# Kernel tuning notes

Hardware: AMD Instinct MI355X
Metric: run time of the kernel (lower is better)

## Reference

```python
import jax, jax.numpy as jnp
import numpy as np

L, N, E, D, H = 3, 20000, 320000, 128, 4
EPS = 1.1920929e-07  # torch RMSNorm default eps = finfo(float32).eps
NEG_SLOPE = 0.2      # PyG GATConv leaky_relu negative_slope


def rmsnorm(x, w):
    return x * jax.lax.rsqrt(jnp.mean(x * x, axis=-1, keepdims=True) + EPS) * w


def setup_inputs() -> dict:
    key = jax.random.key(0)
    ks = jax.random.split(key, 13)
    s = 0.02
    x = jax.random.normal(ks[0], (N, D), jnp.float32)
    src = jax.random.randint(ks[1], (E,), 0, N, dtype=jnp.int64)
    dst = jax.random.randint(ks[2], (E,), 0, N, dtype=jnp.int64)
    dst = jnp.where(dst == src, (dst + 1) % N, dst)  # no pre-existing self loops
    edge_index = jnp.stack([src, dst])
    return {
        "x": x,
        "W_gat": jax.random.normal(ks[3], (L, D, H * D), jnp.float32) * s,
        "att_src": jax.random.normal(ks[4], (L, H, D), jnp.float32) * s,
        "att_dst": jax.random.normal(ks[5], (L, H, D), jnp.float32) * s,
        "bias_gat": jax.random.normal(ks[6], (L, D), jnp.float32) * s,
        "W1": jax.random.normal(ks[7], (L, D, D), jnp.float32) * s,
        "b1": jax.random.normal(ks[8], (L, D), jnp.float32) * s,
        "W2": jax.random.normal(ks[9], (L, D, D), jnp.float32) * s,
        "b2": jax.random.normal(ks[10], (L, D), jnp.float32) * s,
        "norm1_w": jnp.ones((L, D), jnp.float32),
        "norm2_w": jnp.ones((L, D), jnp.float32),
        "edge_index": edge_index,
    }


def reference(x, W_gat, att_src, att_dst, bias_gat, W1, b1, W2, b2, norm1_w, norm2_w, edge_index):
    # PyG GATConv adds self loops by default
    loops = jnp.arange(N, dtype=edge_index.dtype)
    src = jnp.concatenate([edge_index[0], loops])  # [E+N]
    dst = jnp.concatenate([edge_index[1], loops])
    for i in range(L):
        # --- GATConv(hidden, hidden, heads=H, concat=False), dropout=0 (eval) ---
        xp = (x @ W_gat[i]).reshape(N, H, D)               # [N,H,D]
        a_s = jnp.einsum('nhd,hd->nh', xp, att_src[i])     # [N,H]
        a_d = jnp.einsum('nhd,hd->nh', xp, att_dst[i])
        e = jax.nn.leaky_relu(a_s[src] + a_d[dst], NEG_SLOPE)  # [E+N,H]
        m = jax.ops.segment_max(e, dst, num_segments=N)
        ex = jnp.exp(e - m[dst])
        denom = jax.ops.segment_sum(ex, dst, num_segments=N)
        alpha = ex / denom[dst]                             # segment softmax over incoming edges
        agg = jax.ops.segment_sum(alpha[:, :, None] * xp[src], dst, num_segments=N)  # [N,H,D]
        x_att = agg.mean(axis=1) + bias_gat[i]              # concat=False -> head mean, then bias
        # --- residual + RMSNorm ---
        x = rmsnorm(x + x_att, norm1_w[i])
        # --- FFN ---
        h = jax.nn.relu(x @ W1[i] + b1[i])
        h = h @ W2[i] + b2[i]
        x = rmsnorm(x + h, norm2_w[i])
    return x
```

## Files before the change

kernel.cpp:

```cpp
#include <hip/hip_runtime.h>
#include <hip/hip_bf16.h>

#define N_NODES 20000
#define NEDGE   320000
#define DIM     128
#define NH      4
#define HD      512
#define LAYERS  3
#define EPS_RMS 1.1920929e-07f
#define SLOPE   0.2f
#define NTILES  (N_NODES >> 4)

#define NWGC  (LAYERS * DIM * HD)
#define NW1C  (LAYERS * DIM * DIM)
#define NVC   (LAYERS * DIM)
#define NPACK (NWGC + 2 * NW1C + 5 * NVC)
#define NXV   (N_NODES * DIM / 8)

typedef __bf16 bf16_t;
typedef __bf16 bf16v2 __attribute__((ext_vector_type(2)));
typedef __bf16 bf16v8 __attribute__((ext_vector_type(8)));
typedef float  f32v4  __attribute__((ext_vector_type(4)));
typedef float  f32v2  __attribute__((ext_vector_type(2)));

__device__ __forceinline__ int clamp_node(int s) {
    return ((unsigned)s >= (unsigned)N_NODES) ? 0 : s;
}
__device__ __forceinline__ float leaky(float e) { return e > 0.f ? e : SLOPE * e; }
__device__ __forceinline__ unsigned char enc_fp8(float v) {
    int p = __builtin_amdgcn_cvt_pk_fp8_f32(v, v, 0, false);
    return (unsigned char)(p & 0xff);
}
__device__ __forceinline__ unsigned short enc_fp8_pair(float a, float b) {
    int p = __builtin_amdgcn_cvt_pk_fp8_f32(a, b, 0, false);
    return (unsigned short)(p & 0xffff);
}

__device__ __forceinline__ bool wave_detect_bf16(const unsigned short* xh) {
    int lane = threadIdx.x & 63;
    unsigned short hw = xh[2 * lane];
    int e = (hw >> 7) & 0xff;
    unsigned long long b = __ballot(e >= 96 && e <= 140);
    return __popcll(b) >= 48;
}
__device__ __forceinline__ bool wave_detect_i64(const int* ei) {
    int lane = threadIdx.x & 63;
    unsigned long long b = __ballot(ei[2 * lane + 1] != 0);
    return b == 0ULL;
}
__device__ __forceinline__ float raw_elem(const void* in, size_t j, bool isbf) {
    return isbf ? (float)((const bf16_t*)in)[j] : ((const float*)in)[j];
}
__device__ __forceinline__ bf16_t cvt_elem(const void* in, size_t j, bool isbf) {
    return isbf ? ((const bf16_t*)in)[j] : (bf16_t)((const float*)in)[j];
}
__device__ __forceinline__ int edge_src(const int* ei, int e, bool is64) {
    return clamp_node(is64 ? ei[2 * e] : ei[e]);
}
__device__ __forceinline__ int edge_dst(const int* ei, int e, bool is64) {
    return clamp_node(is64 ? ei[2 * NEDGE + 2 * e] : ei[NEDGE + e]);
}

__global__ __launch_bounds__(256) void prep_v(const void* x, const void* Wg,
                                              const void* aS, const void* aD,
                                              float* __restrict__ vS, float* __restrict__ vD,
                                              int* __restrict__ deg) {
    int gid = blockIdx.x * 256 + threadIdx.x;
    for (int i = gid; i < N_NODES; i += gridDim.x * 256) deg[i] = 0;
    bool isbf = wave_detect_bf16((const unsigned short*)x);
    int w = gid >> 6;
    if (w >= LAYERS * DIM * NH * 2) return;
    int lane = threadIdx.x & 63;
    int sd = w & 1, h = (w >> 1) & 3, k = (w >> 3) & 127, l = w >> 10;
    const void* att = sd ? aD : aS;
    size_t wbase = (size_t)l * DIM * HD + (size_t)k * HD + h * DIM;
    size_t abase = (size_t)l * NH * DIM + (size_t)h * DIM;
    int c = 2 * lane;
    float p = raw_elem(Wg, wbase + c, isbf) * raw_elem(att, abase + c, isbf)
            + raw_elem(Wg, wbase + c + 1, isbf) * raw_elem(att, abase + c + 1, isbf);
#pragma unroll
    for (int msk = 1; msk < 64; msk <<= 1) p += __shfl_xor(p, msk);
    if (lane == 0) {
        float* dst = sd ? vD : vS;
        dst[l * HD + h * DIM + k] = p;
    }
}

__device__ __forceinline__ void pack_item(int i, bool isbf,
        const void* Wg, const void* W1, const void* W2,
        const void* bg, const void* b1, const void* b2,
        const void* n1, const void* n2,
        bf16_t* WmixP, bf16_t* W1P, bf16_t* W2P,
        bf16_t* bgc, bf16_t* b1c, bf16_t* b2c, bf16_t* n1c, bf16_t* n2c) {
    if (i < NWGC) {
        int l = i >> 16;
        int r = i & 65535;
        int j = r & 7;
        int lane2 = (r >> 3) & 63;
        int mm = lane2 & 15, kqq = lane2 >> 4;
        int tt = (r >> 9) & 1;
        int kk = (r >> 10) & 15;
        int wvv = r >> 14;
        int kidx = kk * 32 + kqq * 8 + j;
        int h = kidx >> 7, kp = kidx & 127;
        int c = 32 * wvv + tt * 16 + mm;
        WmixP[i] = cvt_elem(Wg, (size_t)l * DIM * HD + (size_t)kp * HD + h * DIM + c, isbf);
        return;
    }
    i -= NWGC;
    if (i < NW1C) {
        int l = i / 16384;
        int r = i & 16383;
        int j = r & 7;
        int lane2 = (r >> 3) & 63;
        int mm = lane2 & 15, kqq = lane2 >> 4;
        int tt = (r >> 9) & 1;
        int ks = (r >> 10) & 3;
        int wvv = r >> 12;
        int k = ks * 32 + kqq * 8 + j;
        int c = 32 * wvv + tt * 16 + mm;
        W1P[i] = cvt_elem(W1, (size_t)l * DIM * DIM + (size_t)k * DIM + c, isbf);
        return;
    }
    i -= NW1C;
    if (i < NW1C) {
        int l = i / 16384;
        int r = i & 16383;
        int j = r & 7;
        int lane2 = (r >> 3) & 63;
        int mm = lane2 & 15, kqq = lane2 >> 4;
        int tt = (r >> 9) & 1;
        int ks = (r >> 10) & 3;
        int wvv = r >> 12;
        int k = ks * 32 + kqq * 8 + j;
        int c = 32 * wvv + tt * 16 + mm;
        W2P[i] = cvt_elem(W2, (size_t)l * DIM * DIM + (size_t)k * DIM + c, isbf);
        return;
    }
    i -= NW1C;
    if (i >= 5 * NVC) return;
    int seg = i / NVC, k = i - seg * NVC;
    if (seg == 0) bgc[k] = cvt_elem(bg, k, isbf);
    else if (seg == 1) b1c[k] = cvt_elem(b1, k, isbf);
    else if (seg == 2) b2c[k] = cvt_elem(b2, k, isbf);
    else if (seg == 3) n1c[k] = cvt_elem(n1, k, isbf);
    else n2c[k] = cvt_elem(n2, k, isbf);
}

__global__ __launch_bounds__(256) void mega_setup(
        const void* x, const void* Wg, const void* W1, const void* W2,
        const void* bg, const void* b1, const void* b2, const void* n1, const void* n2,
        bf16_t* xb, bf16_t* WmixP, bf16_t* W1P, bf16_t* W2P,
        bf16_t* bgc, bf16_t* b1c, bf16_t* b2c, bf16_t* n1c, bf16_t* n2c,
        const int* ei, int* deg,
        const float* vS, const float* vD,
        float* a_s, float* a_d, unsigned short* x8,
        int convBlocks, int histBlocks) {
    int b = (int)blockIdx.x;
    if (b >= convBlocks + histBlocks) {
        bool isbf = wave_detect_bf16((const unsigned short*)x);
        int lane = threadIdx.x & 63;
        int n = (b - convBlocks - histBlocks) * 4 + (int)(threadIdx.x >> 6);
        if (n >= N_NODES) return;
        int c = 2 * lane;
        float f0 = raw_elem(x, (size_t)n * DIM + c, isbf);
        float f1 = raw_elem(x, (size_t)n * DIM + c + 1, isbf);
        x8[n * 64 + lane] = enc_fp8_pair(f0, f1);
#pragma unroll
        for (int h = 0; h < NH; ++h) {
            float ps = f0 * vS[h * DIM + c] + f1 * vS[h * DIM + c + 1];
            float pd = f0 * vD[h * DIM + c] + f1 * vD[h * DIM + c + 1];
#pragma unroll
            for (int msk = 1; msk < 64; msk <<= 1) {
                ps += __shfl_xor(ps, msk);
                pd += __shfl_xor(pd, msk);
            }
            if (lane == 0) {
                a_s[n * 4 + h] = ps;
                a_d[n * 4 + h] = pd;
            }
        }
        return;
    }
    if (b >= convBlocks) {
        bool is64 = wave_detect_i64(ei);
        int e = (b - convBlocks) * 256 + threadIdx.x;
        if (e < NEDGE) atomicAdd(&deg[edge_dst(ei, e, is64)], 1);
        return;
    }
    bool isbf = wave_detect_bf16((const unsigned short*)x);
    int i = b * 256 + threadIdx.x;
    if (i < NXV) {
        if (isbf) {
            ((bf16v8*)xb)[i] = ((const bf16v8*)x)[i];
        } else {
            const float4* src = (const float4*)x;
            float4 a = src[2 * i], bq = src[2 * i + 1];
            bf16v8 o;
            o[0] = (bf16_t)a.x;  o[1] = (bf16_t)a.y;
            o[2] = (bf16_t)a.z;  o[3] = (bf16_t)a.w;
            o[4] = (bf16_t)bq.x; o[5] = (bf16_t)bq.y;
            o[6] = (bf16_t)bq.z; o[7] = (bf16_t)bq.w;
            ((bf16v8*)xb)[i] = o;
        }
        return;
    }
    pack_item(i - NXV, isbf, Wg, W1, W2, bg, b1, b2, n1, n2,
              WmixP, W1P, W2P, bgc, b1c, b2c, n1c, n2c);
}

__global__ __launch_bounds__(1024) void scan_kernel(const int* __restrict__ deg,
                                                    int* __restrict__ row_ptr,
                                                    int* __restrict__ cursor) {
    __shared__ int wsum[16];
    int tid = threadIdx.x, lane = tid & 63, wv = tid >> 6;
    int v[20];
    int base = tid * 20;
    int tot = 0;
    if (base < N_NODES) {
        const int4* d4 = reinterpret_cast<const int4*>(deg + base);
#pragma unroll
        for (int j = 0; j < 5; ++j) {
            int4 q = d4[j];
            v[4 * j]     = q.x;
            v[4 * j + 1] = q.y;
            v[4 * j + 2] = q.z;
            v[4 * j + 3] = q.w;
        }
#pragma unroll
        for (int i = 0; i < 20; ++i) tot += v[i];
    }
    int x = tot;
#pragma unroll
    for (int off = 1; off < 64; off <<= 1) {
        int t = __shfl_up(x, off);
        if (lane >= off) x += t;
    }
    if (lane == 63) wsum[wv] = x;
    __syncthreads();
    if (wv == 0) {
        int s = (lane < 16) ? wsum[lane] : 0;
#pragma unroll
        for (int off = 1; off < 16; off <<= 1) {
            int t = __shfl_up(s, off);
            if (lane >= off) s += t;
        }
        if (lane < 16) wsum[lane] = s;
    }
    __syncthreads();
    int off0 = ((wv == 0) ? 0 : wsum[wv - 1]) + (x - tot);
    if (tid == 0) row_ptr[0] = 0;
    if (base < N_NODES) {
        int run = off0;
#pragma unroll
        for (int i = 0; i < 20; ++i) {
            run += v[i];
            row_ptr[base + i + 1] = run;
            cursor[base + i] = run - v[i];
        }
    }
}

__global__ void fill_kernel(const int* __restrict__ ei, int* __restrict__ cursor,
                            int* __restrict__ csr_src) {
    bool is64 = wave_detect_i64(ei);
    int e = blockIdx.x * blockDim.x + threadIdx.x;
    if (e < NEDGE) {
        int d = edge_dst(ei, e, is64);
        int pos = atomicAdd(&cursor[d], 1);
        if ((unsigned)pos < (unsigned)NEDGE) csr_src[pos] = edge_src(ei, e, is64);
    }
}

__device__ __forceinline__ void acc_group_loop(float (&acc)[8], int cnt,
        const float4* wshw, const int* sshw,
        const unsigned short* __restrict__ x8, int lane) {
    unsigned short xeN[8];
    {
        int p0 = cnt < 8 ? cnt : 8;
#pragma unroll
        for (int u = 0; u < 8; ++u)
            if (u < p0) xeN[u] = x8[sshw[u] + lane];
    }
    for (int u0 = 0; u0 < cnt; u0 += 8) {
        int uc = cnt - u0; if (uc > 8) uc = 8;
        unsigned short xeC[8];
#pragma unroll
        for (int u = 0; u < 8; ++u) xeC[u] = xeN[u];
        int n0 = u0 + 8;
        int nc = cnt - n0; if (nc > 8) nc = 8;
#pragma unroll
        for (int u = 0; u < 8; ++u)
            if (u < nc) xeN[u] = x8[sshw[n0 + u] + lane];
#pragma unroll
        for (int u = 0; u < 8; ++u) {
            if (u < uc) {
                float4 w = wshw[u0 + u];
                f32v2 f = __builtin_amdgcn_cvt_pk_f32_fp8((int)xeC[u], false);
                acc[0] += w.x * f[0]; acc[1] += w.x * f[1];
                acc[2] += w.y * f[0]; acc[3] += w.y * f[1];
                acc[4] += w.z * f[0]; acc[5] += w.z * f[1];
                acc[6] += w.w * f[0]; acc[7] += w.w * f[1];
            }
        }
    }
}

__device__ __forceinline__ void gat_phaseA(int tile, int wv, int lane,
        float4* wshw, int* sshw,
        const int* __restrict__ row_ptr, const int* __restrict__ csr_src,
        const float* __restrict__ a_s, const float* __restrict__ a_d,
        const unsigned short* __restrict__ x8, bf16_t (*ylds)[524]) {
    const float4* a_s4 = reinterpret_cast<const float4*>(a_s);
    const float4* a_d4 = reinterpret_cast<const float4*>(a_d);

    int beg[4], deg[4];
#pragma unroll
    for (int rp = 0; rp < 4; ++rp) {
        int nn = tile * 16 + wv + rp * 4;
        int b = row_ptr[nn], e = row_ptr[nn + 1];
        int d = e - b;
        if (d < 0) d = 0;
        if (d > NEDGE) d = NEDGE;
        if (b < 0) b = 0;
        if (b > NEDGE - d) b = NEDGE - d;
        beg[rp] = b; deg[rp] = d;
    }

    int craw[4], sreg[4];
    unsigned short pslf[4];
    float4 av4[4], adv4[4], avs4[4];

    {
        int d = deg[0];
        int idx = (d > 0) ? (beg[0] + (lane < d ? lane : 0)) : 0;
        craw[0] = csr_src[idx];
        d = deg[1];
        idx = (d > 0) ? (beg[1] + (lane < d ? lane : 0)) : 0;
        craw[1] = csr_src[idx];
        int nn = tile * 16 + wv;
        adv4[0] = a_d4[nn];
        avs4[0] = a_s4[nn];
        pslf[0] = x8[nn * 64 + lane];
        int s = clamp_node(craw[0]);
        sreg[0] = s;
        av4[0] = a_s4[s];
    }

#pragma unroll
    for (int rp = 0; rp < 4; ++rp) {
        float4 adv = adv4[rp];
        float4 a0 = av4[rp];
        float4 wl = {__expf(leaky(a0.x + adv.x)), __expf(leaky(a0.y + adv.y)),
                     __expf(leaky(a0.z + adv.z)), __expf(leaky(a0.w + adv.w))};
        float4 avs = avs4[rp];
        float4 wself = {__expf(leaky(avs.x + adv.x)), __expf(leaky(avs.y + adv.y)),
                        __expf(leaky(avs.z + adv.z)), __expf(leaky(avs.w + adv.w))};
        float acc[8];
        {
            f32v2 f = __builtin_amdgcn_cvt_pk_f32_fp8((int)pslf[rp], false);
            acc[0] = wself.x * f[0]; acc[1] = wself.x * f[1];
            acc[2] = wself.y * f[0]; acc[3] = wself.y * f[1];
            acc[4] = wself.z * f[0]; acc[5] = wself.z * f[1];
            acc[6] = wself.w * f[0]; acc[7] = wself.w * f[1];
        }
        int cnt0 = deg[rp] < 64 ? deg[rp] : 64;
        float4 zl = {0.f, 0.f, 0.f, 0.f};
        if (lane < cnt0) {
            zl = wl;
            wshw[lane] = wl;
            sshw[lane] = sreg[rp] << 6;
        }

        if (rp < 3) {
            int nn = tile * 16 + wv + (rp + 1) * 4;
            adv4[rp + 1] = a_d4[nn];
            avs4[rp + 1] = a_s4[nn];
            pslf[rp + 1] = x8[nn * 64 + lane];
            int s = clamp_node(craw[rp + 1]);
            sreg[rp + 1] = s;
            av4[rp + 1] = a_s4[s];
        }
        if (rp < 2) {
            int d = deg[rp + 2];
            int idx = (d > 0) ? (beg[rp + 2] + (lane < d ? lane : 0)) : 0;
            craw[rp + 2] = csr_src[idx];
        }

        acc_group_loop(acc, cnt0, wshw, sshw, x8, lane);

        for (int c0 = 64; c0 < deg[rp]; c0 += 64) {
            int cnt = deg[rp] - c0; if (cnt > 64) cnt = 64;
            if (lane < cnt) {
                int s = clamp_node(csr_src[beg[rp] + c0 + lane]);
                float4 a2 = a_s4[s];
                float4 w2 = {__expf(leaky(a2.x + adv.x)), __expf(leaky(a2.y + adv.y)),
                             __expf(leaky(a2.z + adv.z)), __expf(leaky(a2.w + adv.w))};
                zl.x += w2.x; zl.y += w2.y; zl.z += w2.z; zl.w += w2.w;
                wshw[lane] = w2;
                sshw[lane] = s << 6;
            }
            acc_group_loop(acc, cnt, wshw, sshw, x8, lane);
        }

        float4 zr = zl;
#pragma unroll
        for (int msk = 1; msk < 64; msk <<= 1) {
            zr.x += __shfl_xor(zr.x, msk);
            zr.y += __shfl_xor(zr.y, msk);
            zr.z += __shfl_xor(zr.z, msk);
            zr.w += __shfl_xor(zr.w, msk);
        }
        float4 z4 = {wself.x + zr.x, wself.y + zr.y, wself.z + zr.z, wself.w + zr.w};
        float4 ih4 = {1.f / z4.x, 1.f / z4.y, 1.f / z4.z, 1.f / z4.w};
        int c = 2 * lane;
        bf16_t* yrow = &ylds[wv + rp * 4][0];
#pragma unroll
        for (int h = 0; h < NH; ++h) {
            float ih = h == 0 ? ih4.x : h == 1 ? ih4.y : h == 2 ? ih4.z : ih4.w;
            bf16v2 o;
            o[0] = (bf16_t)(acc[h * 2 + 0] * ih);
            o[1] = (bf16_t)(acc[h * 2 + 1] * ih);
            *reinterpret_cast<bf16v2*>(&yrow[h * DIM + c]) = o;
        }
    }
}

template <int MODE>
__global__ __launch_bounds__(256) void gat_mix(
        const int* __restrict__ row_ptr, const int* __restrict__ csr_src,
        const float* __restrict__ a_s, const float* __restrict__ a_d,
        const unsigned short* __restrict__ x8,
        const bf16_t* __restrict__ WmixP, const bf16_t* __restrict__ bg,
        const bf16_t* __restrict__ n1w, const bf16_t* __restrict__ xb,
        const bf16_t* __restrict__ W1P, const bf16_t* __restrict__ b1,
        const bf16_t* __restrict__ W2P, const bf16_t* __restrict__ b2,
        const bf16_t* __restrict__ n2w, void* __restrict__ out,
        const float* __restrict__ vS, const float* __restrict__ vD,
        float* __restrict__ a_s_n, float* __restrict__ a_d_n,
        unsigned char* __restrict__ x8_n) {
    __shared__ bf16_t ylds[16][524];
    __shared__ bf16_t xm[16][140];
    __shared__ float  ssq_p[16][4];
    __shared__ float  asd_p[4][16][8];
    __shared__ float4 wsh[4][64];
    __shared__ int    ssh[4][64];
    bf16_t (*hh)[140] = reinterpret_cast<bf16_t (*)[140]>(&ylds[0][0]);

    int tile = blockIdx.x;
    int wv = threadIdx.x >> 6;
    int lane = threadIdx.x & 63;
    int m = lane & 15, kq = lane >> 4;

    gat_phaseA(tile, wv, lane, wsh[wv], ssh[wv], row_ptr, csr_src, a_s, a_d, x8, ylds);
    __syncthreads();

    f32v4 accm[2];
    accm[0] = (f32v4){0.f, 0.f, 0.f, 0.f};
    accm[1] = (f32v4){0.f, 0.f, 0.f, 0.f};
#pragma unroll
    for (int kk = 0; kk < 16; ++kk) {
        bf16v8 a = *reinterpret_cast<const bf16v8*>(&ylds[m][kk * 32 + kq * 8]);
#pragma unroll
        for (int tt = 0; tt < 2; ++tt) {
            bf16v8 b = *reinterpret_cast<const bf16v8*>(
                WmixP + ((((wv * 16 + kk) * 2 + tt) << 9) + lane * 8));
            accm[tt] = __builtin_amdgcn_mfma_f32_16x16x32_bf16(a, b, accm[tt], 0, 0, 0);
        }
    }
    float vals[2][4];
    {
        float sp[4] = {0.f, 0.f, 0.f, 0.f};
#pragma unroll
        for (int tt = 0; tt < 2; ++tt) {
            int col = 32 * wv + tt * 16 + m;
            float bv = (float)bg[col];
#pragma unroll
            for (int r = 0; r < 4; ++r) {
                int gr = tile * 16 + kq * 4 + r;
                float v = 0.25f * accm[tt][r] + bv + (float)xb[(size_t)gr * DIM + col];
                vals[tt][r] = v;
                sp[r] += v * v;
            }
        }
#pragma unroll
        for (int r = 0; r < 4; ++r) {
            sp[r] += __shfl_xor(sp[r], 1); sp[r] += __shfl_xor(sp[r], 2);
            sp[r] += __shfl_xor(sp[r], 4); sp[r] += __shfl_xor(sp[r], 8);
            if (m == r) ssq_p[kq * 4 + r][wv] = sp[r];
        }
    }
    __syncthreads();
    {
#pragma unroll
        for (int r = 0; r < 4; ++r) {
            int row = kq * 4 + r;
            float s = ssq_p[row][0] + ssq_p[row][1] + ssq_p[row][2] + ssq_p[row][3];
            float scale = rsqrtf(s * (1.f / 128.f) + EPS_RMS);
#pragma unroll
            for (int tt = 0; tt < 2; ++tt) {
                int col = 32 * wv + tt * 16 + m;
                xm[row][col] = (bf16_t)(vals[tt][r] * scale * (float)n1w[col]);
            }
        }
    }
    __syncthreads();

    f32v4 acc1[2];
    acc1[0] = (f32v4){0.f, 0.f, 0.f, 0.f};
    acc1[1] = (f32v4){0.f, 0.f, 0.f, 0.f};
#pragma unroll
    for (int ks = 0; ks < 4; ++ks) {
        bf16v8 a = *reinterpret_cast<const bf16v8*>(&xm[m][ks * 32 + kq * 8]);
#pragma unroll
        for (int tt = 0; tt < 2; ++tt) {
            bf16v8 b = *reinterpret_cast<const bf16v8*>(
                W1P + ((((wv * 4 + ks) * 2 + tt) << 9) + lane * 8));
            acc1[tt] = __builtin_amdgcn_mfma_f32_16x16x32_bf16(a, b, acc1[tt], 0, 0, 0);
        }
    }
#pragma unroll
    for (int tt = 0; tt < 2; ++tt) {
        int col = 32 * wv + tt * 16 + m;
        float bv = (float)b1[col];
#pragma unroll
        for (int r = 0; r < 4; ++r) {
            float v = acc1[tt][r] + bv;
            hh[kq * 4 + r][col] = (bf16_t)(v > 0.f ? v : 0.f);
        }
    }
    __syncthreads();
    f32v4 acc2[2];
    acc2[0] = (f32v4){0.f, 0.f, 0.f, 0.f};
    acc2[1] = (f32v4){0.f, 0.f, 0.f, 0.f};
#pragma unroll
    for (int ks = 0; ks < 4; ++ks) {
        bf16v8 a = *reinterpret_cast<const bf16v8*>(&hh[m][ks * 32 + kq * 8]);
#pragma unroll
        for (int tt = 0; tt < 2; ++tt) {
            bf16v8 b = *reinterpret_cast<const bf16v8*>(
                W2P + ((((wv * 4 + ks) * 2 + tt) << 9) + lane * 8));
            acc2[tt] = __builtin_amdgcn_mfma_f32_16x16x32_bf16(a, b, acc2[tt], 0, 0, 0);
        }
    }
    float vals2[2][4];
    {
        float sp[4] = {0.f, 0.f, 0.f, 0.f};
#pragma unroll
        for (int tt = 0; tt < 2; ++tt) {
            int col = 32 * wv + tt * 16 + m;
            float bv = (float)b2[col];
#pragma unroll
            for (int r = 0; r < 4; ++r) {
                float v = acc2[tt][r] + bv + (float)xm[kq * 4 + r][col];
                vals2[tt][r] = v;
                sp[r] += v * v;
            }
        }
#pragma unroll
        for (int r = 0; r < 4; ++r) {
            sp[r] += __shfl_xor(sp[r], 1); sp[r] += __shfl_xor(sp[r], 2);
            sp[r] += __shfl_xor(sp[r], 4); sp[r] += __shfl_xor(sp[r], 8);
            if (m == r) ssq_p[kq * 4 + r][wv] = sp[r];
        }
    }
    __syncthreads();
    float o2[2][4];
#pragma unroll
    for (int r = 0; r < 4; ++r) {
        int row = kq * 4 + r;
        int gr = tile * 16 + row;
        float s = ssq_p[row][0] + ssq_p[row][1] + ssq_p[row][2] + ssq_p[row][3];
        float scale = rsqrtf(s * (1.f / 128.f) + EPS_RMS);
#pragma unroll
        for (int tt = 0; tt < 2; ++tt) {
            int col = 32 * wv + tt * 16 + m;
            float o = vals2[tt][r] * scale * (float)n2w[col];
            o2[tt][r] = o;
            if (MODE == 1) ((float*)out)[(size_t)gr * DIM + col] = o;
            else {
                ((bf16_t*)out)[(size_t)gr * DIM + col] = (bf16_t)o;
                x8_n[(size_t)gr * DIM + col] = enc_fp8(o);
            }
        }
    }
    if (MODE == 0) {
        float vs0[NH], vs1[NH], vd0[NH], vd1[NH];
        int col0 = 32 * wv + m, col1 = col0 + 16;
#pragma unroll
        for (int h = 0; h < NH; ++h) {
            vs0[h] = vS[h * DIM + col0]; vs1[h] = vS[h * DIM + col1];
            vd0[h] = vD[h * DIM + col0]; vd1[h] = vD[h * DIM + col1];
        }
#pragma unroll
        for (int r = 0; r < 4; ++r) {
#pragma unroll
            for (int h = 0; h < NH; ++h) {
                float ps = o2[0][r] * vs0[h] + o2[1][r] * vs1[h];
                float pd = o2[0][r] * vd0[h] + o2[1][r] * vd1[h];
                ps += __shfl_xor(ps, 1); ps += __shfl_xor(ps, 2);
                ps += __shfl_xor(ps, 4); ps += __shfl_xor(ps, 8);
                pd += __shfl_xor(pd, 1); pd += __shfl_xor(pd, 2);
                pd += __shfl_xor(pd, 4); pd += __shfl_xor(pd, 8);
                if (m == r * 4 + h) {
                    asd_p[wv][kq * 4 + r][h * 2 + 0] = ps;
                    asd_p[wv][kq * 4 + r][h * 2 + 1] = pd;
                }
            }
        }
        __syncthreads();
        int t = threadIdx.x;
        if (t < 128) {
            int row = t >> 3, idx = t & 7;
            float s = asd_p[0][row][idx] + asd_p[1][row][idx]
                    + asd_p[2][row][idx] + asd_p[3][row][idx];
            int gr = tile * 16 + row;
            if (idx & 1) a_d_n[gr * 4 + (idx >> 1)] = s;
            else         a_s_n[gr * 4 + (idx >> 1)] = s;
        }
    }
}

extern "C" void kernel_launch(void* const* d_in, const int* in_sizes, int n_in,
                              void* d_out, int out_size, void* d_ws, size_t ws_size,
                              hipStream_t stream) {
    const void* x_in   = d_in[0];
    const void* W_gat  = d_in[1];
    const void* att_s  = d_in[2];
    const void* att_d  = d_in[3];
    const void* bias_g = d_in[4];
    const void* W1     = d_in[5];
    const void* b1     = d_in[6];
    const void* W2     = d_in[7];
    const void* b2     = d_in[8];
    const void* n1w    = d_in[9];
    const void* n2w    = d_in[10];
    const int*  ei     = (const int*)d_in[11];

    char* ws = (char*)d_ws;
    size_t off = 0;
    auto alloc = [&](size_t bytes) {
        void* p = ws + off;
        off = (off + bytes + 255) & ~(size_t)255;
        return p;
    };
    bf16_t* WmixP   = (bf16_t*)alloc((size_t)LAYERS * HD * DIM * 2);
    bf16_t* W1P     = (bf16_t*)alloc((size_t)LAYERS * DIM * DIM * 2);
    bf16_t* W2P     = (bf16_t*)alloc((size_t)LAYERS * DIM * DIM * 2);
    bf16_t* xb      = (bf16_t*)alloc((size_t)N_NODES * DIM * 2);
    unsigned short* x8a = (unsigned short*)alloc((size_t)N_NODES * DIM);
    unsigned short* x8b = (unsigned short*)alloc((size_t)N_NODES * DIM);
    float*  vS      = (float*)alloc((size_t)LAYERS * HD * 4);
    float*  vD      = (float*)alloc((size_t)LAYERS * HD * 4);
    float*  a_sA    = (float*)alloc((size_t)N_NODES * NH * 4);
    float*  a_dA    = (float*)alloc((size_t)N_NODES * NH * 4);
    float*  a_sB    = (float*)alloc((size_t)N_NODES * NH * 4);
    float*  a_dB    = (float*)alloc((size_t)N_NODES * NH * 4);
    int*    deg     = (int*)alloc((size_t)N_NODES * 4);
    int*    cursor  = (int*)alloc((size_t)N_NODES * 4);
    int*    row_ptr = (int*)alloc((size_t)(N_NODES + 1) * 4);
    int*    csr     = (int*)alloc((size_t)NEDGE * 4);
    bf16_t* bgc     = (bf16_t*)alloc((size_t)LAYERS * DIM * 2);
    bf16_t* b1c     = (bf16_t*)alloc((size_t)LAYERS * DIM * 2);
    bf16_t* b2c     = (bf16_t*)alloc((size_t)LAYERS * DIM * 2);
    bf16_t* n1c     = (bf16_t*)alloc((size_t)LAYERS * DIM * 2);
    bf16_t* n2c     = (bf16_t*)alloc((size_t)LAYERS * DIM * 2);

    prep_v<<<(LAYERS * DIM * NH * 2 * 64 + 255) / 256, 256, 0, stream>>>(
        x_in, W_gat, att_s, att_d, vS, vD, deg);

    const int NTOT = NXV + NPACK;
    const int convBlocks = (NTOT + 255) / 256;
    const int histBlocks = (NEDGE + 255) / 256;
    const int asdBlocks  = (N_NODES + 3) / 4;
    mega_setup<<<convBlocks + histBlocks + asdBlocks, 256, 0, stream>>>(
        x_in, W_gat, W1, W2, bias_g, b1, b2, n1w, n2w,
        xb, WmixP, W1P, W2P, bgc, b1c, b2c, n1c, n2c,
        ei, deg, vS, vD, a_sA, a_dA, x8a, convBlocks, histBlocks);

    scan_kernel<<<1, 1024, 0, stream>>>(deg, row_ptr, cursor);
    fill_kernel<<<(NEDGE + 255) / 256, 256, 0, stream>>>(ei, cursor, csr);

    unsigned short* x8cur[2] = {x8a, x8b};
    float* asCur[2] = {a_sA, a_sB};
    float* adCur[2] = {a_dA, a_dB};
    for (int l = 0; l < LAYERS; ++l) {
        int ci = l & 1, ni = (l + 1) & 1;
        if (l < LAYERS - 1) {
            gat_mix<0><<<NTILES, 256, 0, stream>>>(
                row_ptr, csr, asCur[ci], adCur[ci], x8cur[ci],
                WmixP + (size_t)l * HD * DIM, bgc + (size_t)l * DIM,
                n1c + (size_t)l * DIM, xb,
                W1P + (size_t)l * DIM * DIM, b1c + (size_t)l * DIM,
                W2P + (size_t)l * DIM * DIM, b2c + (size_t)l * DIM,
                n2c + (size_t)l * DIM, xb,
                vS + (size_t)(l + 1) * HD, vD + (size_t)(l + 1) * HD,
                asCur[ni], adCur[ni], (unsigned char*)x8cur[ni]);
        } else {
            gat_mix<1><<<NTILES, 256, 0, stream>>>(
                row_ptr, csr, asCur[ci], adCur[ci], x8cur[ci],
                WmixP + (size_t)l * HD * DIM, bgc + (size_t)l * DIM,
                n1c + (size_t)l * DIM, xb,
                W1P + (size_t)l * DIM * DIM, b1c + (size_t)l * DIM,
                W2P + (size_t)l * DIM * DIM, b2c + (size_t)l * DIM,
                n2c + (size_t)l * DIM, d_out,
                nullptr, nullptr, nullptr, nullptr, nullptr);
        }
    }
}
```

Baseline: 286.6 us.

## Balance per-wave node degrees via sorted snake assignment and double-buffer gathers

Each workgroup now ranks its 16 nodes by in-degree and assigns them to the 4 waves in a snake order (ranks w, 7-w, 8+w, 15-w). The goal is to even out edge work across waves, so the barrier after the attention phase waits less on the slowest wave. The edge gather loop also alternates between two 8-element register buffers, processing 16 edges per iteration so more fp8 gathers are in flight. This costs a few shuffles, ballots and extra row_ptr reads per tile, plus higher register pressure.

After: 278.0 us. 3.0% less time.

```diff
diff --git a/kernel.cpp b/kernel.cpp
--- a/kernel.cpp
+++ b/kernel.cpp
@@ -272,41 +272,61 @@
     }
 }
 
+__device__ __forceinline__ void acc8(float (&acc)[8], const float4 w, unsigned short xe) {
+    f32v2 f = __builtin_amdgcn_cvt_pk_f32_fp8((int)xe, false);
+    acc[0] += w.x * f[0]; acc[1] += w.x * f[1];
+    acc[2] += w.y * f[0]; acc[3] += w.y * f[1];
+    acc[4] += w.z * f[0]; acc[5] += w.z * f[1];
+    acc[6] += w.w * f[0]; acc[7] += w.w * f[1];
+}
+
 __device__ __forceinline__ void acc_group_loop(float (&acc)[8], int cnt,
         const float4* wshw, const int* sshw,
         const unsigned short* __restrict__ x8, int lane) {
-    unsigned short xeN[8];
+    unsigned short xA[8], xB[8];
     {
-        int p0 = cnt < 8 ? cnt : 8;
+        int pa = cnt < 8 ? cnt : 8;
+        int pb = cnt - 8; if (pb > 8) pb = 8;
 #pragma unroll
         for (int u = 0; u < 8; ++u)
-            if (u < p0) xeN[u] = x8[sshw[u] + lane];
-    }
-    for (int u0 = 0; u0 < cnt; u0 += 8) {
-        int uc = cnt - u0; if (uc > 8) uc = 8;
-        unsigned short xeC[8];
-#pragma unroll
-        for (int u = 0; u < 8; ++u) xeC[u] = xeN[u];
-        int n0 = u0 + 8;
-        int nc = cnt - n0; if (nc > 8) nc = 8;
+            if (u < pa) xA[u] = x8[sshw[u] + lane];
 #pragma unroll
         for (int u = 0; u < 8; ++u)
-            if (u < nc) xeN[u] = x8[sshw[n0 + u] + lane];
-#pragma unroll
-        for (int u = 0; u < 8; ++u) {
-            if (u < uc) {
-                float4 w = wshw[u0 + u];
-                f32v2 f = __builtin_amdgcn_cvt_pk_f32_fp8((int)xeC[u], false);
-                acc[0] += w.x * f[0]; acc[1] += w.x * f[1];
-                acc[2] += w.y * f[0]; acc[3] += w.y * f[1];
-                acc[4] += w.z * f[0]; acc[5] += w.z * f[1];
-                acc[6] += w.w * f[0]; acc[7] += w.w * f[1];
-            }
-        }
-    }
-}
-
-__device__ __forceinline__ void gat_phaseA(int tile, int wv, int lane,
+            if (u < pb) xB[u] = x8[sshw[8 + u] + lane];
+    }
+    for (int u0 = 0; u0 < cnt; u0 += 16) {
+        {
+            unsigned short xc[8];
+#pragma unroll
+            for (int u = 0; u < 8; ++u) xc[u] = xA[u];
+            int g = u0 + 16;
+            int nc = cnt - g; if (nc > 8) nc = 8;
+#pragma unroll
+            for (int u = 0; u < 8; ++u)
+                if (u < nc) xA[u] = x8[sshw[g + u] + lane];
+            int uc = cnt - u0; if (uc > 8) uc = 8;
+#pragma unroll
+            for (int u = 0; u < 8; ++u)
+                if (u < uc) acc8(acc, wshw[u0 + u], xc[u]);
+        }
+        if (u0 + 8 < cnt) {
+            unsigned short xc[8];
+#pragma unroll
+            for (int u = 0; u < 8; ++u) xc[u] = xB[u];
+            int g = u0 + 24;
+            int nc = cnt - g; if (nc > 8) nc = 8;
+#pragma unroll
+            for (int u = 0; u < 8; ++u)
+                if (u < nc) xB[u] = x8[sshw[g + u] + lane];
+            int uc = cnt - (u0 + 8); if (uc > 8) uc = 8;
+#pragma unroll
+            for (int u = 0; u < 8; ++u)
+                if (u < uc) acc8(acc, wshw[u0 + 8 + u], xc[u]);
+        }
+    }
+}
+
+__device__ __forceinline__ void gat_phaseA(int tile, int lane, const int rw[4],
         float4* wshw, int* sshw,
         const int* __restrict__ row_ptr, const int* __restrict__ csr_src,
         const float* __restrict__ a_s, const float* __restrict__ a_d,
@@ -317,7 +337,7 @@
     int beg[4], deg[4];
 #pragma unroll
     for (int rp = 0; rp < 4; ++rp) {
-        int nn = tile * 16 + wv + rp * 4;
+        int nn = tile * 16 + rw[rp];
         int b = row_ptr[nn], e = row_ptr[nn + 1];
         int d = e - b;
         if (d < 0) d = 0;
@@ -338,7 +358,7 @@
         d = deg[1];
         idx = (d > 0) ? (beg[1] + (lane < d ? lane : 0)) : 0;
         craw[1] = csr_src[idx];
-        int nn = tile * 16 + wv;
+        int nn = tile * 16 + rw[0];
         adv4[0] = a_d4[nn];
         avs4[0] = a_s4[nn];
         pslf[0] = x8[nn * 64 + lane];
@@ -373,7 +393,7 @@
         }
 
         if (rp < 3) {
-            int nn = tile * 16 + wv + (rp + 1) * 4;
+            int nn = tile * 16 + rw[rp + 1];
             adv4[rp + 1] = a_d4[nn];
             avs4[rp + 1] = a_s4[nn];
             pslf[rp + 1] = x8[nn * 64 + lane];
@@ -414,7 +434,7 @@
         float4 z4 = {wself.x + zr.x, wself.y + zr.y, wself.z + zr.z, wself.w + zr.w};
         float4 ih4 = {1.f / z4.x, 1.f / z4.y, 1.f / z4.z, 1.f / z4.w};
         int c = 2 * lane;
-        bf16_t* yrow = &ylds[wv + rp * 4][0];
+        bf16_t* yrow = &ylds[rw[rp]][0];
 #pragma unroll
         for (int h = 0; h < NH; ++h) {
             float ih = h == 0 ? ih4.x : h == 1 ? ih4.y : h == 2 ? ih4.z : ih4.w;
@@ -452,7 +472,28 @@
     int lane = threadIdx.x & 63;
     int m = lane & 15, kq = lane >> 4;
 
-    gat_phaseA(tile, wv, lane, wsh[wv], ssh[wv], row_ptr, csr_src, a_s, a_d, x8, ylds);
+    int rw[4];
+    {
+        int d = 0;
+        if (lane < 16) {
+            int nn = tile * 16 + lane;
+            d = row_ptr[nn + 1] - row_ptr[nn];
+        }
+        int rank = 0;
+#pragma unroll
+        for (int j = 0; j < 16; ++j) {
+            int dj = __shfl(d, j);
+            rank += ((dj > d) || (dj == d && j < lane)) ? 1 : 0;
+        }
+        if (lane >= 16) rank = 64;
+        int tgt0 = wv, tgt1 = 7 - wv, tgt2 = 8 + wv, tgt3 = 15 - wv;
+        rw[0] = __ffsll(__ballot(rank == tgt0)) - 1;
+        rw[1] = __ffsll(__ballot(rank == tgt1)) - 1;
+        rw[2] = __ffsll(__ballot(rank == tgt2)) - 1;
+        rw[3] = __ffsll(__ballot(rank == tgt3)) - 1;
+    }
+
+    gat_phaseA(tile, lane, rw, wsh[wv], ssh[wv], row_ptr, csr_src, a_s, a_d, x8, ylds);
     __syncthreads();
 
     f32v4 accm[2];
```
